# Kernel tuning notes

Hardware: AMD Instinct MI355X
Metric: run time of the kernel (lower is better)

Reference implementation:

```python
import jax, jax.numpy as jnp
import numpy as np

D_MODEL = 1024
N_HEADS = 16
D_K = D_MODEL // N_HEADS
B, S = 2, 2048


def setup_inputs() -> dict:
    key = jax.random.key(0)
    ks = jax.random.split(key, 12)
    scale = 1.0 / np.sqrt(D_MODEL)
    inp = {
        "query": jax.random.normal(ks[0], (B, S, D_MODEL), jnp.float32),
        "key": jax.random.normal(ks[1], (B, S, D_MODEL), jnp.float32),
        "value": jax.random.normal(ks[2], (B, S, D_MODEL), jnp.float32),
        "mask": jnp.tril(jnp.ones((S, S), dtype=bool))[None, None],  # (1,1,S,S) causal
        "W_q": jax.random.normal(ks[3], (D_MODEL, D_MODEL), jnp.float32) * scale,
        "b_q": jnp.zeros((D_MODEL,), jnp.float32),
        "W_k": jax.random.normal(ks[4], (D_MODEL, D_MODEL), jnp.float32) * scale,
        "b_k": jnp.zeros((D_MODEL,), jnp.float32),
        "W_v": jax.random.normal(ks[5], (D_MODEL, D_MODEL), jnp.float32) * scale,
        "b_v": jnp.zeros((D_MODEL,), jnp.float32),
        "W_o": jax.random.normal(ks[6], (D_MODEL, D_MODEL), jnp.float32) * scale,
        "b_o": jnp.zeros((D_MODEL,), jnp.float32),
    }
    return inp


def reference(query, key, value, mask, W_q, b_q, W_k, b_k, W_v, b_v, W_o, b_o):
    b = query.shape[0]
    # Linear projections (torch Linear: x @ W.T + b), split into heads -> (b,h,s,d_k)
    def proj(x, W, bias):
        y = x @ W.T + bias
        return y.reshape(b, -1, N_HEADS, D_K).transpose(0, 2, 1, 3)

    q = proj(query, W_q, b_q)
    k = proj(key, W_k, b_k)
    v = proj(value, W_v, b_v)

    # scores: (b,h,sq,sk)
    scores = jnp.einsum("bhqd,bhkd->bhqk", q, k) / jnp.sqrt(jnp.float32(D_K)).astype(q.dtype)
    scores = jnp.where(mask, scores, jnp.finfo(scores.dtype).min)
    attn = jax.nn.softmax(scores, axis=-1)
    out = jnp.einsum("bhqk,bhkd->bhqd", attn, v)  # (b,h,sq,d_k)
    out = out.transpose(0, 2, 1, 3).reshape(b, -1, D_MODEL)
    return out @ W_o.T + b_o
```

## Files before the change

### kernel.cpp

```cpp
#include <hip/hip_runtime.h>
#include <hip/hip_bf16.h>
#include <stdint.h>

#define D_MODEL 1024
#define NH 16
#define DK 64
#define BB 2
#define SS 2048
#define MROWS (BB*SS)

typedef __attribute__((ext_vector_type(8))) short bf16x8;
typedef __attribute__((ext_vector_type(4))) float f32x4;

__device__ __forceinline__ short to_bf16(float f) {
  __hip_bfloat16 h = __float2bfloat16(f);
  union { __hip_bfloat16 b; short s; } u; u.b = h; return u.s;
}

__device__ __forceinline__ f32x4 mfma16(bf16x8 a, bf16x8 b, f32x4 c) {
  return __builtin_amdgcn_mfma_f32_16x16x32_bf16(a, b, c, 0, 0, 0);
}

__device__ __forceinline__ void gload_lds16(const void* g, void* l) {
  __builtin_amdgcn_global_load_lds(
      (const __attribute__((address_space(1))) unsigned int*)g,
      (__attribute__((address_space(3))) unsigned int*)l,
      16, 0, 0);
}

__device__ __forceinline__ float max3f(float a, float b, float c) {
  return fmaxf(fmaxf(a, b), c);
}

__global__ __launch_bounds__(256) void cvt3(const float* __restrict__ a,
                                            const float* __restrict__ b,
                                            const float* __restrict__ c,
                                            short* __restrict__ oa,
                                            short* __restrict__ ob,
                                            short* __restrict__ oc) {
  const int z = blockIdx.z;
  const float* x = z == 0 ? a : z == 1 ? b : c;
  short* y = z == 0 ? oa : z == 1 ? ob : oc;
  const int i = (blockIdx.x * 256 + threadIdx.x) * 4;
  const float4 v = *(const float4*)(x + i);
  short4 o;
  o.x = to_bf16(v.x); o.y = to_bf16(v.y); o.z = to_bf16(v.z); o.w = to_bf16(v.w);
  *(short4*)(y + i) = o;
}

__global__ __launch_bounds__(256) void cvt4(const float* __restrict__ a,
                                            const float* __restrict__ b,
                                            const float* __restrict__ c,
                                            const float* __restrict__ d,
                                            short* __restrict__ oa,
                                            short* __restrict__ ob,
                                            short* __restrict__ oc,
                                            short* __restrict__ od) {
  const int z = blockIdx.z;
  const float* x = z == 0 ? a : z == 1 ? b : z == 2 ? c : d;
  short* y = z == 0 ? oa : z == 1 ? ob : z == 2 ? oc : od;
  const int i = (blockIdx.x * 256 + threadIdx.x) * 4;
  const float4 v = *(const float4*)(x + i);
  short4 o;
  o.x = to_bf16(v.x); o.y = to_bf16(v.y); o.z = to_bf16(v.z); o.w = to_bf16(v.w);
  *(short4*)(y + i) = o;
}

__global__ __launch_bounds__(256) void gemm_qkv(const short* __restrict__ Xq,
                                                const short* __restrict__ Xk,
                                                const short* __restrict__ Xv,
                                                const short* __restrict__ Wq,
                                                const short* __restrict__ Wk,
                                                const short* __restrict__ Wv,
                                                const float* __restrict__ bq,
                                                const float* __restrict__ bk,
                                                const float* __restrict__ bv,
                                                short* __restrict__ Qh,
                                                short* __restrict__ Kh,
                                                short* __restrict__ VT) {
  constexpr int K = 1024, NSTEP = K / 32;
  __shared__ short As[2][128 * 32];
  __shared__ short Bs[2][128 * 32];
  const int z = blockIdx.z;
  const short* A    = z == 0 ? Xq : z == 1 ? Xk : Xv;
  const short* Wt   = z == 0 ? Wq : z == 1 ? Wk : Wv;
  const float* bias = z == 0 ? bq : z == 1 ? bk : bv;

  const int tid = threadIdx.x;
  const int w = tid >> 6, lane = tid & 63;
  const int m0 = blockIdx.x * 128, n0 = blockIdx.y * 128;
  const int wm = w >> 1, wn = w & 1;
  const int fr = lane & 15, fg = lane >> 4;
  const int srow = tid >> 2, scol = (tid & 3) * 8;

  f32x4 acc[4][4] = {};

#define QKV_STAGE(buf, k0)                                                    \
  do {                                                                        \
    _Pragma("unroll") for (int i = 0; i < 2; ++i) {                           \
      const int row = i * 64 + srow;                                          \
      gload_lds16(A  + (size_t)(m0 + row) * K + (k0) + scol,                  \
                  &As[buf][row * 32 + scol]);                                 \
      gload_lds16(Wt + (size_t)(n0 + row) * K + (k0) + scol,                  \
                  &Bs[buf][row * 32 + scol]);                                 \
    }                                                                         \
  } while (0)

  QKV_STAGE(0, 0);
  asm volatile("s_waitcnt vmcnt(0)" ::: "memory");
  __syncthreads();

  for (int t = 0; t < NSTEP; ++t) {
    const int cur = t & 1;
    if (t + 1 < NSTEP) QKV_STAGE(cur ^ 1, (t + 1) * 32);

    bf16x8 af[4], bfr[4];
#pragma unroll
    for (int i = 0; i < 4; ++i) {
      af[i]  = *(const bf16x8*)(&As[cur][(wm * 64 + i * 16 + fr) * 32 + fg * 8]);
      bfr[i] = *(const bf16x8*)(&Bs[cur][(wn * 64 + i * 16 + fr) * 32 + fg * 8]);
    }
    __builtin_amdgcn_s_setprio(1);
#pragma unroll
    for (int mi = 0; mi < 4; ++mi)
#pragma unroll
      for (int ni = 0; ni < 4; ++ni)
        acc[mi][ni] = mfma16(af[mi], bfr[ni], acc[mi][ni]);
    __builtin_amdgcn_s_setprio(0);

    asm volatile("s_waitcnt vmcnt(0)" ::: "memory");
    __syncthreads();
  }
#undef QKV_STAGE

  const float scale = (z == 0) ? 0.18033688011112042f : 1.0f;
#pragma unroll
  for (int mi = 0; mi < 4; ++mi)
#pragma unroll
    for (int ni = 0; ni < 4; ++ni) {
      const int col = n0 + wn * 64 + ni * 16 + fr;
      const float bval = bias[col];
      const int h = col >> 6, d = col & 63;
#pragma unroll
      for (int r = 0; r < 4; ++r) {
        const int row = m0 + wm * 64 + mi * 16 + fg * 4 + r;
        const float val = (acc[mi][ni][r] + bval) * scale;
        const int b = row >> 11, s = row & (SS - 1);
        if (z < 2) {
          short* dst = (z == 0) ? Qh : Kh;
          dst[((size_t)(b * NH + h) * SS + s) * DK + d] = to_bf16(val);
        } else {
          VT[((size_t)(b * NH + h) * DK + d) * SS + s] = to_bf16(val);
        }
      }
    }
}

__global__ __launch_bounds__(256) void gemm_out(const short* __restrict__ A,
                                                const short* __restrict__ Wt,
                                                const float* __restrict__ bias,
                                                float* __restrict__ Y) {
  constexpr int K = 1024, NSTEP = K / 32;
  __shared__ short As[2][128 * 32];
  __shared__ short Bs[2][64 * 32];
  const int tid = threadIdx.x;
  const int w = tid >> 6, lane = tid & 63;
  const int m0 = blockIdx.x * 128, n0 = blockIdx.y * 64;
  const int wm = w >> 1, wn = w & 1;
  const int fr = lane & 15, fg = lane >> 4;
  const int srow = tid >> 2, scol = (tid & 3) * 8;

  f32x4 acc[4][2] = {};

#define OUT_STAGE(buf, k0)                                                    \
  do {                                                                        \
    _Pragma("unroll") for (int i = 0; i < 2; ++i) {                           \
      const int row = i * 64 + srow;                                          \
      gload_lds16(A + (size_t)(m0 + row) * K + (k0) + scol,                   \
                  &As[buf][row * 32 + scol]);                                 \
    }                                                                         \
    if (srow < 64)                                                            \
      gload_lds16(Wt + (size_t)(n0 + srow) * K + (k0) + scol,                 \
                  &Bs[buf][srow * 32 + scol]);                                \
  } while (0)

  OUT_STAGE(0, 0);
  asm volatile("s_waitcnt vmcnt(0)" ::: "memory");
  __syncthreads();

  for (int t = 0; t < NSTEP; ++t) {
    const int cur = t & 1;
    if (t + 1 < NSTEP) OUT_STAGE(cur ^ 1, (t + 1) * 32);

    bf16x8 af[4], bfr[2];
#pragma unroll
    for (int i = 0; i < 4; ++i)
      af[i] = *(const bf16x8*)(&As[cur][(wm * 64 + i * 16 + fr) * 32 + fg * 8]);
#pragma unroll
    for (int i = 0; i < 2; ++i)
      bfr[i] = *(const bf16x8*)(&Bs[cur][(wn * 32 + i * 16 + fr) * 32 + fg * 8]);
    __builtin_amdgcn_s_setprio(1);
#pragma unroll
    for (int mi = 0; mi < 4; ++mi)
#pragma unroll
      for (int ni = 0; ni < 2; ++ni)
        acc[mi][ni] = mfma16(af[mi], bfr[ni], acc[mi][ni]);
    __builtin_amdgcn_s_setprio(0);

    asm volatile("s_waitcnt vmcnt(0)" ::: "memory");
    __syncthreads();
  }
#undef OUT_STAGE

#pragma unroll
  for (int mi = 0; mi < 4; ++mi)
#pragma unroll
    for (int ni = 0; ni < 2; ++ni) {
      const int col = n0 + wn * 32 + ni * 16 + fr;
      const float bval = bias[col];
#pragma unroll
      for (int r = 0; r < 4; ++r) {
        const int row = m0 + wm * 64 + mi * 16 + fg * 4 + r;
        Y[(size_t)row * D_MODEL + col] = acc[mi][ni][r] + bval;
      }
    }
}

__global__ __launch_bounds__(256) void attn_kernel(const short* __restrict__ Qh,
                                                   const short* __restrict__ Kh,
                                                   const short* __restrict__ VT,
                                                   short* __restrict__ AO) {
  __shared__ short Ks[3][64 * 64];
  __shared__ short Vs[3][64 * 64];
  __shared__ short P_lds[4][16 * 64];

  const int tid = threadIdx.x, w = tid >> 6, lane = tid & 63;
  const int fr = lane & 15, fg = lane >> 4;
  const int kr = fg * 4;
  const int swz = (fr & 7) << 4;

  const int bid = blockIdx.x;
  const int lid = ((bid & 7) << 6) | (bid >> 3);
  const int bh = lid >> 4;
  const int j = lid & 15;
  const int b = bh >> 4, h = bh & 15;

  const short* Qp = Qh + (size_t)bh * SS * DK;
  const short* Kp = Kh + (size_t)bh * SS * DK;
  const short* Vp = VT + (size_t)bh * DK * SS;

  const int sc_c = tid & 7;
  const int sc_r = tid >> 3;

  const int T0 = j + 1;

  bf16x8 qf[2];
#pragma unroll
  for (int hh = 0; hh < 2; ++hh)
    qf[hh] = *(const bf16x8*)(Qp + (size_t)(j * 64 + w * 16 + fr) * DK + hh * 32 + fg * 8);

  const short onev = (fr == 0) ? (short)0x3F80 : (short)0;
  const bf16x8 af4 = {onev, onev, onev, onev, onev, onev, onev, onev};

  f32x4 o[5] = {};
  float m_run = -1e30f;
  f32x4 stA[4], stB[4];

#define KK0(g) ((((g) < T0) ? (g) : ((g) - T0)) * 64)
#define STAGE_KV(buf, kk0)                                                    \
  do {                                                                        \
    _Pragma("unroll") for (int p = 0; p < 2; ++p) {                           \
      const int row = p * 32 + sc_r;                                          \
      const int sc = sc_c ^ (row & 7);                                        \
      gload_lds16(Kp + (size_t)((kk0) + row) * DK + sc * 8,                   \
                  &Ks[buf][row * 64 + sc_c * 8]);                             \
      gload_lds16(Vp + (size_t)row * SS + (kk0) + sc * 8,                     \
                  &Vs[buf][row * 64 + sc_c * 8]);                             \
    }                                                                         \
  } while (0)

  auto softmax_pv = [&](int bufPrev) {
    float p0 = max3f(stB[0][0], stB[0][1], stB[0][2]);
    float p1 = max3f(stB[0][3], stB[1][0], stB[1][1]);
    float p2 = max3f(stB[1][2], stB[1][3], stB[2][0]);
    float p3 = max3f(stB[2][1], stB[2][2], stB[2][3]);
    float p4 = max3f(stB[3][0], stB[3][1], stB[3][2]);
    float pmax = fmaxf(max3f(p0, p1, p2), max3f(p3, p4, stB[3][3]));
    pmax = fmaxf(pmax, __shfl_xor(pmax, 16));
    pmax = fmaxf(pmax, __shfl_xor(pmax, 32));

    if (!__all(pmax <= m_run + 11.0f)) {
      const float mn = fmaxf(m_run, pmax);
      const float al = __builtin_amdgcn_exp2f(m_run - mn);
      m_run = mn;
#pragma unroll
      for (int t = 0; t < 5; ++t)
#pragma unroll
        for (int r = 0; r < 4; ++r) o[t][r] *= al;
    }

    char* base = (char*)P_lds[w];
#pragma unroll
    for (int kt = 0; kt < 4; ++kt) {
      short4 sv;
      sv.x = to_bf16(__builtin_amdgcn_exp2f(stB[kt][0] - m_run));
      sv.y = to_bf16(__builtin_amdgcn_exp2f(stB[kt][1] - m_run));
      sv.z = to_bf16(__builtin_amdgcn_exp2f(stB[kt][2] - m_run));
      sv.w = to_bf16(__builtin_amdgcn_exp2f(stB[kt][3] - m_run));
      *(short4*)(base + ((fr * 128 + kt * 32 + fg * 8) ^ swz)) = sv;
    }
    asm volatile("s_waitcnt lgkmcnt(0)" ::: "memory");

    const char* VsB = (const char*)Vs[bufPrev];
    __builtin_amdgcn_s_setprio(1);
#pragma unroll
    for (int c = 0; c < 2; ++c) {
      const bf16x8 pf = *(const bf16x8*)((const char*)P_lds[w] +
                                         ((fr * 128 + c * 64 + fg * 16) ^ swz));
#pragma unroll
      for (int t = 0; t < 4; ++t) {
        const bf16x8 vfb = *(const bf16x8*)(VsB + (t * 16 + fr) * 128 +
                                            ((c * 64 + fg * 16) ^ swz));
        o[t] = mfma16(vfb, pf, o[t]);
      }
      o[4] = mfma16(af4, pf, o[4]);
    }
    __builtin_amdgcn_s_setprio(0);
  };

  auto store_o = [&](int qbase) {
    const float l = __shfl(o[4][0], fr);
    const float inv = 1.0f / l;
    const int s = qbase + w * 16 + fr;
#pragma unroll
    for (int t = 0; t < 4; ++t) {
      short4 ov = {to_bf16(o[t][0] * inv), to_bf16(o[t][1] * inv),
                   to_bf16(o[t][2] * inv), to_bf16(o[t][3] * inv)};
      *(short4*)(AO + (size_t)(b * SS + s) * D_MODEL + h * 64 + t * 16 + kr) = ov;
    }
  };

  STAGE_KV(0, 0);
  STAGE_KV(1, KK0(1));
  asm volatile("s_waitcnt vmcnt(0)" ::: "memory");
  __syncthreads();

  for (int g = 0; g < 33; ++g) {
    if (g == T0) {
#pragma unroll
      for (int hh = 0; hh < 2; ++hh)
        qf[hh] = *(const bf16x8*)(Qp + (size_t)((31 - j) * 64 + w * 16 + fr) * DK + hh * 32 + fg * 8);
    }

    {
      const char* KsB = (const char*)Ks[g % 3];
      __builtin_amdgcn_s_setprio(1);
#pragma unroll
      for (int kt = 0; kt < 4; ++kt) {
        const bf16x8 k0f = *(const bf16x8*)(KsB + (kt * 16 + fr) * 128 + ((fg * 16) ^ swz));
        const bf16x8 k1f = *(const bf16x8*)(KsB + (kt * 16 + fr) * 128 + ((64 + fg * 16) ^ swz));
        f32x4 z = {};
        z = mfma16(k0f, qf[0], z);
        z = mfma16(k1f, qf[1], z);
        stA[kt] = z;
      }
      __builtin_amdgcn_s_setprio(0);
    }
    if (g == T0 - 1 || g == 32) {
#pragma unroll
      for (int kt = 0; kt < 4; ++kt)
#pragma unroll
        for (int r = 0; r < 4; ++r)
          if (kt * 16 + kr + r > w * 16 + fr) stA[kt][r] = -1e30f;
    }

    if (g > 0) {
      softmax_pv((g - 1) % 3);
      if (g == T0) {
        store_o(j * 64);
#pragma unroll
        for (int t = 0; t < 5; ++t)
#pragma unroll
          for (int r = 0; r < 4; ++r) o[t][r] = 0.f;
        m_run = -1e30f;
      }
    }

#pragma unroll
    for (int kt = 0; kt < 4; ++kt) stB[kt] = stA[kt];

    asm volatile("s_waitcnt vmcnt(0)" ::: "memory");
    __syncthreads();
    if (g + 2 <= 32) STAGE_KV((g + 2) % 3, KK0(g + 2));
  }

  softmax_pv(32 % 3);
  store_o((31 - j) * 64);
#undef STAGE_KV
#undef KK0
}

extern "C" void kernel_launch(void* const* d_in, const int* in_sizes, int n_in,
                              void* d_out, int out_size, void* d_ws, size_t ws_size,
                              hipStream_t stream) {
  const float* q  = (const float*)d_in[0];
  const float* k  = (const float*)d_in[1];
  const float* v  = (const float*)d_in[2];
  const float* Wq = (const float*)d_in[4];
  const float* bq = (const float*)d_in[5];
  const float* Wk = (const float*)d_in[6];
  const float* bk = (const float*)d_in[7];
  const float* Wv = (const float*)d_in[8];
  const float* bv = (const float*)d_in[9];
  const float* Wo = (const float*)d_in[10];
  const float* bo = (const float*)d_in[11];

  char* ws = (char*)d_ws;
  const size_t MB = 1u << 20;
  short* Xq = (short*)(ws + 0 * MB);
  short* Xk = (short*)(ws + 8 * MB);
  short* Xv = (short*)(ws + 16 * MB);
  short* Bq = (short*)(ws + 24 * MB);
  short* Bk = (short*)(ws + 26 * MB);
  short* Bv = (short*)(ws + 28 * MB);
  short* Bo = (short*)(ws + 30 * MB);
  short* Qh = (short*)(ws + 32 * MB);
  short* Kh = (short*)(ws + 40 * MB);
  short* VT = (short*)(ws + 48 * MB);
  short* AO = (short*)(ws + 56 * MB);

  cvt3<<<dim3(MROWS * D_MODEL / 1024, 1, 3), 256, 0, stream>>>(q, k, v, Xq, Xk, Xv);
  cvt4<<<dim3(D_MODEL * D_MODEL / 1024, 1, 4), 256, 0, stream>>>(Wq, Wk, Wv, Wo, Bq, Bk, Bv, Bo);

  gemm_qkv<<<dim3(MROWS / 128, D_MODEL / 128, 3), 256, 0, stream>>>(
      Xq, Xk, Xv, Bq, Bk, Bv, bq, bk, bv, Qh, Kh, VT);

  attn_kernel<<<dim3(512), 256, 0, stream>>>(Qh, Kh, VT, AO);

  gemm_out<<<dim3(MROWS / 128, D_MODEL / 64), 256, 0, stream>>>(AO, Bo, bo, (float*)d_out);
}
```

Baseline: 123.2 us.

## Deepen GEMM prefetch, transpose V via LDS, widen attention KV tiles

The QKV and output GEMMs move from double to triple LDS buffering with a two-step prefetch and partial vmcnt waits, so global loads overlap more with MFMA work. The V projection epilogue now transposes through LDS and writes VT as coalesced 16-byte stores instead of scattered 2-byte stores. The attention kernel processes 128-key tiles, halving loop iterations. It stages K and V separately in double buffers and adjusts the causal masking offsets to match. The new wait and barrier placement risks LDS read-before-load hazards and raises register pressure from the larger score arrays.

Measured after the change: 120.1 us. 1.03x faster.

```diff
diff --git a/kernel.cpp b/kernel.cpp
--- a/kernel.cpp
+++ b/kernel.cpp
@@ -79,8 +79,7 @@
                                                 short* __restrict__ Kh,
                                                 short* __restrict__ VT) {
   constexpr int K = 1024, NSTEP = K / 32;
-  __shared__ short As[2][128 * 32];
-  __shared__ short Bs[2][128 * 32];
+  __shared__ __align__(16) char pool[49152];
   const int z = blockIdx.z;
   const short* A    = z == 0 ? Xq : z == 1 ? Xk : Xv;
   const short* Wt   = z == 0 ? Wq : z == 1 ? Wk : Wv;
@@ -97,28 +96,32 @@
 
 #define QKV_STAGE(buf, k0)                                                    \
   do {                                                                        \
+    short* As_ = (short*)(pool + (buf) * 16384);                              \
+    short* Bs_ = (short*)(pool + (buf) * 16384 + 8192);                       \
     _Pragma("unroll") for (int i = 0; i < 2; ++i) {                           \
       const int row = i * 64 + srow;                                          \
       gload_lds16(A  + (size_t)(m0 + row) * K + (k0) + scol,                  \
-                  &As[buf][row * 32 + scol]);                                 \
+                  As_ + row * 32 + scol);                                     \
       gload_lds16(Wt + (size_t)(n0 + row) * K + (k0) + scol,                  \
-                  &Bs[buf][row * 32 + scol]);                                 \
+                  Bs_ + row * 32 + scol);                                     \
     }                                                                         \
   } while (0)
 
   QKV_STAGE(0, 0);
-  asm volatile("s_waitcnt vmcnt(0)" ::: "memory");
+  QKV_STAGE(1, 32);
+  asm volatile("s_waitcnt vmcnt(4)" ::: "memory");
   __syncthreads();
 
   for (int t = 0; t < NSTEP; ++t) {
-    const int cur = t & 1;
-    if (t + 1 < NSTEP) QKV_STAGE(cur ^ 1, (t + 1) * 32);
-
+    if (t + 2 < NSTEP) QKV_STAGE((t + 2) % 3, (t + 2) * 32);
+
+    const short* Ab = (const short*)(pool + (t % 3) * 16384);
+    const short* Bb = (const short*)(pool + (t % 3) * 16384 + 8192);
     bf16x8 af[4], bfr[4];
 #pragma unroll
     for (int i = 0; i < 4; ++i) {
-      af[i]  = *(const bf16x8*)(&As[cur][(wm * 64 + i * 16 + fr) * 32 + fg * 8]);
-      bfr[i] = *(const bf16x8*)(&Bs[cur][(wn * 64 + i * 16 + fr) * 32 + fg * 8]);
+      af[i]  = *(const bf16x8*)(Ab + (wm * 64 + i * 16 + fr) * 32 + fg * 8);
+      bfr[i] = *(const bf16x8*)(Bb + (wn * 64 + i * 16 + fr) * 32 + fg * 8);
     }
     __builtin_amdgcn_s_setprio(1);
 #pragma unroll
@@ -128,32 +131,57 @@
         acc[mi][ni] = mfma16(af[mi], bfr[ni], acc[mi][ni]);
     __builtin_amdgcn_s_setprio(0);
 
-    asm volatile("s_waitcnt vmcnt(0)" ::: "memory");
+    if (t + 2 < NSTEP)
+      asm volatile("s_waitcnt vmcnt(4)" ::: "memory");
+    else
+      asm volatile("s_waitcnt vmcnt(0)" ::: "memory");
     __syncthreads();
   }
 #undef QKV_STAGE
 
-  const float scale = (z == 0) ? 0.18033688011112042f : 1.0f;
-#pragma unroll
-  for (int mi = 0; mi < 4; ++mi)
-#pragma unroll
-    for (int ni = 0; ni < 4; ++ni) {
-      const int col = n0 + wn * 64 + ni * 16 + fr;
-      const float bval = bias[col];
+  if (z < 2) {
+    const float scale = (z == 0) ? 0.18033688011112042f : 1.0f;
+    short* dst = (z == 0) ? Qh : Kh;
+#pragma unroll
+    for (int mi = 0; mi < 4; ++mi)
+#pragma unroll
+      for (int ni = 0; ni < 4; ++ni) {
+        const int col = n0 + wn * 64 + ni * 16 + fr;
+        const float bval = bias[col];
+        const int h = col >> 6, d = col & 63;
+#pragma unroll
+        for (int r = 0; r < 4; ++r) {
+          const int row = m0 + wm * 64 + mi * 16 + fg * 4 + r;
+          const float val = (acc[mi][ni][r] + bval) * scale;
+          const int b = row >> 11, s = row & (SS - 1);
+          dst[((size_t)(b * NH + h) * SS + s) * DK + d] = to_bf16(val);
+        }
+      }
+  } else {
+    short* trs = (short*)pool;
+#pragma unroll
+    for (int mi = 0; mi < 4; ++mi)
+#pragma unroll
+      for (int ni = 0; ni < 4; ++ni) {
+        const int dl = wn * 64 + ni * 16 + fr;
+        const int s0 = wm * 64 + mi * 16 + fg * 4;
+        const float bval = bias[n0 + dl];
+        short4 sv = {to_bf16(acc[mi][ni][0] + bval), to_bf16(acc[mi][ni][1] + bval),
+                     to_bf16(acc[mi][ni][2] + bval), to_bf16(acc[mi][ni][3] + bval)};
+        *(short4*)(trs + dl * 128 + (s0 ^ ((dl & 7) << 3))) = sv;
+      }
+    __syncthreads();
+    const int b = m0 >> 11, sbase = m0 & (SS - 1);
+#pragma unroll
+    for (int rep = 0; rep < 8; ++rep) {
+      const int dl = (tid >> 4) + rep * 16;
+      const int s0 = (tid & 15) * 8;
+      const bf16x8 vv = *(const bf16x8*)(trs + dl * 128 + (s0 ^ ((dl & 7) << 3)));
+      const int col = n0 + dl;
       const int h = col >> 6, d = col & 63;
-#pragma unroll
-      for (int r = 0; r < 4; ++r) {
-        const int row = m0 + wm * 64 + mi * 16 + fg * 4 + r;
-        const float val = (acc[mi][ni][r] + bval) * scale;
-        const int b = row >> 11, s = row & (SS - 1);
-        if (z < 2) {
-          short* dst = (z == 0) ? Qh : Kh;
-          dst[((size_t)(b * NH + h) * SS + s) * DK + d] = to_bf16(val);
-        } else {
-          VT[((size_t)(b * NH + h) * DK + d) * SS + s] = to_bf16(val);
-        }
-      }
-    }
+      *(bf16x8*)(VT + ((size_t)(b * NH + h) * DK + d) * SS + sbase + s0) = vv;
+    }
+  }
 }
 
 __global__ __launch_bounds__(256) void gemm_out(const short* __restrict__ A,
@@ -161,8 +189,7 @@
                                                 const float* __restrict__ bias,
                                                 float* __restrict__ Y) {
   constexpr int K = 1024, NSTEP = K / 32;
-  __shared__ short As[2][128 * 32];
-  __shared__ short Bs[2][64 * 32];
+  __shared__ __align__(16) char pool[36864];
   const int tid = threadIdx.x;
   const int w = tid >> 6, lane = tid & 63;
   const int m0 = blockIdx.x * 128, n0 = blockIdx.y * 64;
@@ -174,31 +201,34 @@
 
 #define OUT_STAGE(buf, k0)                                                    \
   do {                                                                        \
+    short* As_ = (short*)(pool + (buf) * 12288);                              \
+    short* Bs_ = (short*)(pool + (buf) * 12288 + 8192);                       \
     _Pragma("unroll") for (int i = 0; i < 2; ++i) {                           \
       const int row = i * 64 + srow;                                          \
       gload_lds16(A + (size_t)(m0 + row) * K + (k0) + scol,                   \
-                  &As[buf][row * 32 + scol]);                                 \
+                  As_ + row * 32 + scol);                                     \
     }                                                                         \
-    if (srow < 64)                                                            \
-      gload_lds16(Wt + (size_t)(n0 + srow) * K + (k0) + scol,                 \
-                  &Bs[buf][srow * 32 + scol]);                                \
+    gload_lds16(Wt + (size_t)(n0 + srow) * K + (k0) + scol,                   \
+                Bs_ + srow * 32 + scol);                                      \
   } while (0)
 
   OUT_STAGE(0, 0);
-  asm volatile("s_waitcnt vmcnt(0)" ::: "memory");
+  OUT_STAGE(1, 32);
+  asm volatile("s_waitcnt vmcnt(3)" ::: "memory");
   __syncthreads();
 
   for (int t = 0; t < NSTEP; ++t) {
-    const int cur = t & 1;
-    if (t + 1 < NSTEP) OUT_STAGE(cur ^ 1, (t + 1) * 32);
-
+    if (t + 2 < NSTEP) OUT_STAGE((t + 2) % 3, (t + 2) * 32);
+
+    const short* Ab = (const short*)(pool + (t % 3) * 12288);
+    const short* Bb = (const short*)(pool + (t % 3) * 12288 + 8192);
     bf16x8 af[4], bfr[2];
 #pragma unroll
     for (int i = 0; i < 4; ++i)
-      af[i] = *(const bf16x8*)(&As[cur][(wm * 64 + i * 16 + fr) * 32 + fg * 8]);
+      af[i] = *(const bf16x8*)(Ab + (wm * 64 + i * 16 + fr) * 32 + fg * 8);
 #pragma unroll
     for (int i = 0; i < 2; ++i)
-      bfr[i] = *(const bf16x8*)(&Bs[cur][(wn * 32 + i * 16 + fr) * 32 + fg * 8]);
+      bfr[i] = *(const bf16x8*)(Bb + (wn * 32 + i * 16 + fr) * 32 + fg * 8);
     __builtin_amdgcn_s_setprio(1);
 #pragma unroll
     for (int mi = 0; mi < 4; ++mi)
@@ -207,7 +237,10 @@
         acc[mi][ni] = mfma16(af[mi], bfr[ni], acc[mi][ni]);
     __builtin_amdgcn_s_setprio(0);
 
-    asm volatile("s_waitcnt vmcnt(0)" ::: "memory");
+    if (t + 2 < NSTEP)
+      asm volatile("s_waitcnt vmcnt(3)" ::: "memory");
+    else
+      asm volatile("s_waitcnt vmcnt(0)" ::: "memory");
     __syncthreads();
   }
 #undef OUT_STAGE
@@ -230,8 +263,8 @@
                                                    const short* __restrict__ Kh,
                                                    const short* __restrict__ VT,
                                                    short* __restrict__ AO) {
-  __shared__ short Ks[3][64 * 64];
-  __shared__ short Vs[3][64 * 64];
+  __shared__ short Ks[2][2][64 * 64];
+  __shared__ short Vs[2][2][64 * 64];
   __shared__ short P_lds[4][16 * 64];
 
   const int tid = threadIdx.x, w = tid >> 6, lane = tid & 63;
@@ -252,7 +285,9 @@
   const int sc_c = tid & 7;
   const int sc_r = tid >> 3;
 
-  const int T0 = j + 1;
+  const int T0 = (j + 2) >> 1;
+  const int koff0 = j * 64 - (T0 - 1) * 128;
+  const int koff1 = (31 - j) * 64 - (16 - T0) * 128;
 
   bf16x8 qf[2];
 #pragma unroll
@@ -264,28 +299,37 @@
 
   f32x4 o[5] = {};
   float m_run = -1e30f;
-  f32x4 stA[4], stB[4];
-
-#define KK0(g) ((((g) < T0) ? (g) : ((g) - T0)) * 64)
-#define STAGE_KV(buf, kk0)                                                    \
+  f32x4 stA[8], stB[8];
+
+#define KK0(g) ((((g) < T0) ? (g) : ((g) - T0)) * 128)
+#define STAGE_K(buf, kk0)                                                     \
   do {                                                                        \
+    _Pragma("unroll") for (int hf = 0; hf < 2; ++hf)                          \
     _Pragma("unroll") for (int p = 0; p < 2; ++p) {                           \
       const int row = p * 32 + sc_r;                                          \
       const int sc = sc_c ^ (row & 7);                                        \
-      gload_lds16(Kp + (size_t)((kk0) + row) * DK + sc * 8,                   \
-                  &Ks[buf][row * 64 + sc_c * 8]);                             \
-      gload_lds16(Vp + (size_t)row * SS + (kk0) + sc * 8,                     \
-                  &Vs[buf][row * 64 + sc_c * 8]);                             \
+      gload_lds16(Kp + (size_t)((kk0) + hf * 64 + row) * DK + sc * 8,         \
+                  &Ks[buf][hf][row * 64 + sc_c * 8]);                         \
     }                                                                         \
   } while (0)
+#define STAGE_V(buf, kk0)                                                     \
+  do {                                                                        \
+    _Pragma("unroll") for (int hf = 0; hf < 2; ++hf)                          \
+    _Pragma("unroll") for (int p = 0; p < 2; ++p) {                           \
+      const int row = p * 32 + sc_r;                                          \
+      const int sc = sc_c ^ (row & 7);                                        \
+      gload_lds16(Vp + (size_t)row * SS + (kk0) + hf * 64 + sc * 8,           \
+                  &Vs[buf][hf][row * 64 + sc_c * 8]);                         \
+    }                                                                         \
+  } while (0)
 
   auto softmax_pv = [&](int bufPrev) {
-    float p0 = max3f(stB[0][0], stB[0][1], stB[0][2]);
-    float p1 = max3f(stB[0][3], stB[1][0], stB[1][1]);
-    float p2 = max3f(stB[1][2], stB[1][3], stB[2][0]);
-    float p3 = max3f(stB[2][1], stB[2][2], stB[2][3]);
-    float p4 = max3f(stB[3][0], stB[3][1], stB[3][2]);
-    float pmax = fmaxf(max3f(p0, p1, p2), max3f(p3, p4, stB[3][3]));
+    float mm[8];
+#pragma unroll
+    for (int i = 0; i < 8; ++i)
+      mm[i] = fmaxf(fmaxf(stB[i][0], stB[i][1]), fmaxf(stB[i][2], stB[i][3]));
+    float pmax = fmaxf(max3f(mm[0], mm[1], mm[2]),
+                       fmaxf(max3f(mm[3], mm[4], mm[5]), fmaxf(mm[6], mm[7])));
     pmax = fmaxf(pmax, __shfl_xor(pmax, 16));
     pmax = fmaxf(pmax, __shfl_xor(pmax, 32));
 
@@ -299,33 +343,36 @@
         for (int r = 0; r < 4; ++r) o[t][r] *= al;
     }
 
-    char* base = (char*)P_lds[w];
-#pragma unroll
-    for (int kt = 0; kt < 4; ++kt) {
-      short4 sv;
-      sv.x = to_bf16(__builtin_amdgcn_exp2f(stB[kt][0] - m_run));
-      sv.y = to_bf16(__builtin_amdgcn_exp2f(stB[kt][1] - m_run));
-      sv.z = to_bf16(__builtin_amdgcn_exp2f(stB[kt][2] - m_run));
-      sv.w = to_bf16(__builtin_amdgcn_exp2f(stB[kt][3] - m_run));
-      *(short4*)(base + ((fr * 128 + kt * 32 + fg * 8) ^ swz)) = sv;
-    }
-    asm volatile("s_waitcnt lgkmcnt(0)" ::: "memory");
-
-    const char* VsB = (const char*)Vs[bufPrev];
-    __builtin_amdgcn_s_setprio(1);
-#pragma unroll
-    for (int c = 0; c < 2; ++c) {
-      const bf16x8 pf = *(const bf16x8*)((const char*)P_lds[w] +
-                                         ((fr * 128 + c * 64 + fg * 16) ^ swz));
-#pragma unroll
-      for (int t = 0; t < 4; ++t) {
-        const bf16x8 vfb = *(const bf16x8*)(VsB + (t * 16 + fr) * 128 +
-                                            ((c * 64 + fg * 16) ^ swz));
-        o[t] = mfma16(vfb, pf, o[t]);
-      }
-      o[4] = mfma16(af4, pf, o[4]);
-    }
-    __builtin_amdgcn_s_setprio(0);
+#pragma unroll
+    for (int hf = 0; hf < 2; ++hf) {
+      char* base = (char*)P_lds[w];
+#pragma unroll
+      for (int kt = 0; kt < 4; ++kt) {
+        short4 sv;
+        sv.x = to_bf16(__builtin_amdgcn_exp2f(stB[hf * 4 + kt][0] - m_run));
+        sv.y = to_bf16(__builtin_amdgcn_exp2f(stB[hf * 4 + kt][1] - m_run));
+        sv.z = to_bf16(__builtin_amdgcn_exp2f(stB[hf * 4 + kt][2] - m_run));
+        sv.w = to_bf16(__builtin_amdgcn_exp2f(stB[hf * 4 + kt][3] - m_run));
+        *(short4*)(base + ((fr * 128 + kt * 32 + fg * 8) ^ swz)) = sv;
+      }
+      asm volatile("s_waitcnt lgkmcnt(0)" ::: "memory");
+
+      const char* VsB = (const char*)Vs[bufPrev][hf];
+      __builtin_amdgcn_s_setprio(1);
+#pragma unroll
+      for (int c = 0; c < 2; ++c) {
+        const bf16x8 pf = *(const bf16x8*)((const char*)P_lds[w] +
+                                           ((fr * 128 + c * 64 + fg * 16) ^ swz));
+#pragma unroll
+        for (int t = 0; t < 4; ++t) {
+          const bf16x8 vfb = *(const bf16x8*)(VsB + (t * 16 + fr) * 128 +
+                                              ((c * 64 + fg * 16) ^ swz));
+          o[t] = mfma16(vfb, pf, o[t]);
+        }
+        o[4] = mfma16(af4, pf, o[4]);
+      }
+      __builtin_amdgcn_s_setprio(0);
+    }
   };
 
   auto store_o = [&](int qbase) {
@@ -340,42 +387,51 @@
     }
   };
 
-  STAGE_KV(0, 0);
-  STAGE_KV(1, KK0(1));
+  STAGE_K(0, 0);
+  STAGE_V(0, 0);
   asm volatile("s_waitcnt vmcnt(0)" ::: "memory");
   __syncthreads();
 
-  for (int g = 0; g < 33; ++g) {
+  for (int g = 0; g < 17; ++g) {
     if (g == T0) {
 #pragma unroll
       for (int hh = 0; hh < 2; ++hh)
         qf[hh] = *(const bf16x8*)(Qp + (size_t)((31 - j) * 64 + w * 16 + fr) * DK + hh * 32 + fg * 8);
     }
 
+    if (g + 1 < 17) STAGE_K((g + 1) & 1, KK0(g + 1));
+
     {
-      const char* KsB = (const char*)Ks[g % 3];
       __builtin_amdgcn_s_setprio(1);
 #pragma unroll
-      for (int kt = 0; kt < 4; ++kt) {
-        const bf16x8 k0f = *(const bf16x8*)(KsB + (kt * 16 + fr) * 128 + ((fg * 16) ^ swz));
-        const bf16x8 k1f = *(const bf16x8*)(KsB + (kt * 16 + fr) * 128 + ((64 + fg * 16) ^ swz));
-        f32x4 z = {};
-        z = mfma16(k0f, qf[0], z);
-        z = mfma16(k1f, qf[1], z);
-        stA[kt] = z;
+      for (int hf = 0; hf < 2; ++hf) {
+        const char* KsB = (const char*)Ks[g & 1][hf];
+#pragma unroll
+        for (int kt = 0; kt < 4; ++kt) {
+          const bf16x8 k0f = *(const bf16x8*)(KsB + (kt * 16 + fr) * 128 + ((fg * 16) ^ swz));
+          const bf16x8 k1f = *(const bf16x8*)(KsB + (kt * 16 + fr) * 128 + ((64 + fg * 16) ^ swz));
+          f32x4 zz = {};
+          zz = mfma16(k0f, qf[0], zz);
+          zz = mfma16(k1f, qf[1], zz);
+          stA[hf * 4 + kt] = zz;
+        }
       }
       __builtin_amdgcn_s_setprio(0);
     }
-    if (g == T0 - 1 || g == 32) {
-#pragma unroll
-      for (int kt = 0; kt < 4; ++kt)
-#pragma unroll
-        for (int r = 0; r < 4; ++r)
-          if (kt * 16 + kr + r > w * 16 + fr) stA[kt][r] = -1e30f;
+    if (g == T0 - 1 || g == 16) {
+      const int koff = (g == 16) ? koff1 : koff0;
+#pragma unroll
+      for (int hf = 0; hf < 2; ++hf)
+#pragma unroll
+        for (int kt = 0; kt < 4; ++kt)
+#pragma unroll
+          for (int r = 0; r < 4; ++r)
+            if (hf * 64 + kt * 16 + kr + r > koff + w * 16 + fr)
+              stA[hf * 4 + kt][r] = -1e30f;
     }
 
     if (g > 0) {
-      softmax_pv((g - 1) % 3);
+      softmax_pv((g - 1) & 1);
       if (g == T0) {
         store_o(j * 64);
 #pragma unroll
@@ -387,16 +443,21 @@
     }
 
 #pragma unroll
-    for (int kt = 0; kt < 4; ++kt) stB[kt] = stA[kt];
-
-    asm volatile("s_waitcnt vmcnt(0)" ::: "memory");
+    for (int i = 0; i < 8; ++i) stB[i] = stA[i];
+
     __syncthreads();
-    if (g + 2 <= 32) STAGE_KV((g + 2) % 3, KK0(g + 2));
+    if (g + 1 < 17) {
+      STAGE_V((g + 1) & 1, KK0(g + 1));
+      asm volatile("s_waitcnt vmcnt(4)" ::: "memory");
+    } else {
+      asm volatile("s_waitcnt vmcnt(0)" ::: "memory");
+    }
   }
 
-  softmax_pv(32 % 3);
+  softmax_pv(16 & 1);
   store_o((31 - j) * 64);
-#undef STAGE_KV
+#undef STAGE_K
+#undef STAGE_V
 #undef KK0
 }
 
```
